# Optimization experiments

Measured on AMD Instinct MI355X. Metric: run time of the kernel, lower is better.

## Reference

```python
import math
import jax, jax.numpy as jnp
import numpy as np

C, NH, NL, NP, NLAYERS, FFN = 256, 8, 3, 4, 6, 1024
DH = C // NH
SHAPES = ((64, 64), (32, 32), (16, 16))  # (H,W) for res3, res4, res5
SIZES = [h * w for h, w in SHAPES]
STARTS = np.cumsum([0] + SIZES[:-1]).tolist()
EPS = 1e-5


def _sin_pe(H, W):
    d = C // 4
    y = jnp.arange(H, dtype=jnp.float32)[:, None]
    x = jnp.arange(W, dtype=jnp.float32)[None, :]
    div = jnp.exp(jnp.arange(d, dtype=jnp.float32) * (-math.log(10000.0) / d))[:, None, None]
    pe = jnp.concatenate([
        jnp.broadcast_to(jnp.sin(y * div), (d, H, W)),
        jnp.broadcast_to(jnp.cos(y * div), (d, H, W)),
        jnp.broadcast_to(jnp.sin(x * div), (d, H, W)),
        jnp.broadcast_to(jnp.cos(x * div), (d, H, W)),
    ], axis=0)  # (C,H,W)
    return pe.reshape(C, H * W).T  # (HW, C)


def _ref_points():
    pts = []
    for H, W in SHAPES:
        y = jnp.linspace(0.5 / H, 1.0 - 0.5 / H, H)
        x = jnp.linspace(0.5 / W, 1.0 - 0.5 / W, W)
        ry, rx = jnp.meshgrid(y, x, indexing='ij')
        pts.append(jnp.stack([rx.ravel(), ry.ravel()], -1))
    return jnp.concatenate(pts, 0)[None, :, None, :]  # (1,N,1,2), same per level


def _layernorm(x, g, b):
    mu = x.mean(-1, keepdims=True)
    v = ((x - mu) ** 2).mean(-1, keepdims=True)
    return (x - mu) * jax.lax.rsqrt(v + EPS) * g + b


def _bilinear(v, loc, H, W):
    # v: (B,HW,NH,DH); loc: (B,N,NH,NP,2) in [0,1]; grid_sample align_corners=False, zero pad
    B, N = loc.shape[0], loc.shape[1]
    x = loc[..., 0] * W - 0.5
    y = loc[..., 1] * H - 0.5
    x0 = jnp.floor(x); y0 = jnp.floor(y)
    wx = x - x0; wy = y - y0
    x0i = x0.astype(jnp.int32); y0i = y0.astype(jnp.int32)
    v_t = jnp.transpose(v, (0, 2, 1, 3))  # (B,NH,HW,DH)

    def corner(xi, yi, w):
        valid = (xi >= 0) & (xi < W) & (yi >= 0) & (yi < H)
        idx = jnp.clip(yi, 0, H - 1) * W + jnp.clip(xi, 0, W - 1)  # (B,N,NH,NP)
        idx = jnp.transpose(idx, (0, 2, 1, 3)).reshape(B, NH, N * NP)
        g = jnp.take_along_axis(v_t, idx[..., None], axis=2)  # (B,NH,N*NP,DH)
        g = g.reshape(B, NH, N, NP, DH).transpose(0, 2, 1, 3, 4)
        return g * (w * valid)[..., None]

    return (corner(x0i, y0i, (1 - wx) * (1 - wy))
            + corner(x0i + 1, y0i, wx * (1 - wy))
            + corner(x0i, y0i + 1, (1 - wx) * wy)
            + corner(x0i + 1, y0i + 1, wx * wy))


def _forward(res2, res3, res4, res5, level_embed, off_W, off_b, aw_W, aw_b, val_W, val_b,
             out_W, out_b, ln1_g, ln1_b, fc1_W, fc1_b, fc2_W, fc2_b, ln2_g, ln2_b,
             lat_W, lat_b, sm_W, sm_b, gn_g, gn_b):
    feats = [res3, res4, res5]
    B = res3.shape[0]
    flat = jnp.concatenate(
        [f.reshape(B, C, -1).transpose(0, 2, 1) + level_embed[i] for i, f in enumerate(feats)], 1)
    pe = jnp.concatenate([_sin_pe(H, W) for H, W in SHAPES], 0)[None]  # (1,N,C)
    ref = _ref_points()  # (1,N,1,2)
    normalizer = jnp.array([[W, H] for H, W in SHAPES], jnp.float32)  # (NL,2) as (W,H)
    N = flat.shape[1]

    x = flat
    for l in range(NLAYERS):
        q = x + pe
        value = (x @ val_W[l].T + val_b[l]).reshape(B, N, NH, DH)
        off = (q @ off_W[l].T + off_b[l]).reshape(B, N, NH, NL, NP, 2)
        aw = jax.nn.softmax((q @ aw_W[l].T + aw_b[l]).reshape(B, N, NH, NL * NP), -1)
        aw = aw.reshape(B, N, NH, NL, NP)
        loc = ref[:, :, None, :, None, :] + off / normalizer[None, None, None, :, None, :]
        attn = jnp.zeros((B, N, NH, DH), x.dtype)
        for li, (H, W) in enumerate(SHAPES):
            v_l = value[:, STARTS[li]:STARTS[li] + SIZES[li]]
            samp = _bilinear(v_l, loc[:, :, :, li], H, W)  # (B,N,NH,NP,DH)
            attn = attn + jnp.einsum('bnhpd,bnhp->bnhd', samp, aw[:, :, :, li])
        attn = attn.reshape(B, N, C) @ out_W[l].T + out_b[l]
        x = _layernorm(x + attn, ln1_g[l], ln1_b[l])
        h = jax.nn.relu(x @ fc1_W[l].T + fc1_b[l]) @ fc2_W[l].T + fc2_b[l]
        x = _layernorm(x + h, ln2_g[l], ln2_b[l])

    outs = []
    for li, (H, W) in enumerate(SHAPES):
        tok = x[:, STARTS[li]:STARTS[li] + SIZES[li]]
        outs.append(tok.transpose(0, 2, 1).reshape(B, C, H, W))
    o3, o4, o5 = outs

    r2_lat = jnp.einsum('bchw,oc->bohw', res2, lat_W) + lat_b[None, :, None, None]
    Hr, Wr = res2.shape[2], res2.shape[3]
    r3_up = jax.image.resize(o3, (B, C, Hr, Wr), method='bilinear')
    s = jax.lax.conv_general_dilated(r2_lat + r3_up, sm_W, (1, 1), ((1, 1), (1, 1)),
                                     dimension_numbers=('NCHW', 'OIHW', 'NCHW'))
    s = s + sm_b[None, :, None, None]
    # GroupNorm(32, C)
    g = s.reshape(B, 32, C // 32, Hr, Wr)
    mu = g.mean((2, 3, 4), keepdims=True)
    var = jnp.var(g, axis=(2, 3, 4), keepdims=True)
    g = (g - mu) * jax.lax.rsqrt(var + EPS)
    s = g.reshape(B, C, Hr, Wr) * gn_g[None, :, None, None] + gn_b[None, :, None, None]
    s = jax.nn.gelu(s, approximate=False)
    return s, o3, o4, o5


def setup_inputs() -> dict:
    key = jax.random.key(0)
    ks = jax.random.split(key, 16)
    def rn(k, shape, s=0.02):
        return jax.random.normal(k, shape, jnp.float32) * s
    B = 2
    L = NLAYERS
    return {
        'res2': jax.random.normal(ks[0], (B, C, 128, 128), jnp.float32),
        'res3': jax.random.normal(ks[1], (B, C, 64, 64), jnp.float32),
        'res4': jax.random.normal(ks[2], (B, C, 32, 32), jnp.float32),
        'res5': jax.random.normal(ks[3], (B, C, 16, 16), jnp.float32),
        'level_embed': rn(ks[4], (NL, C)),
        'off_W': rn(ks[5], (L, NH * NL * NP * 2, C)), 'off_b': jnp.zeros((L, NH * NL * NP * 2)),
        'aw_W': rn(ks[6], (L, NH * NL * NP, C)), 'aw_b': jnp.zeros((L, NH * NL * NP)),
        'val_W': rn(ks[7], (L, C, C)), 'val_b': jnp.zeros((L, C)),
        'out_W': rn(ks[8], (L, C, C)), 'out_b': jnp.zeros((L, C)),
        'ln1_g': jnp.ones((L, C)), 'ln1_b': jnp.zeros((L, C)),
        'fc1_W': rn(ks[9], (L, FFN, C)), 'fc1_b': jnp.zeros((L, FFN)),
        'fc2_W': rn(ks[10], (L, C, FFN)), 'fc2_b': jnp.zeros((L, C)),
        'ln2_g': jnp.ones((L, C)), 'ln2_b': jnp.zeros((L, C)),
        'lat_W': rn(ks[11], (C, C)), 'lat_b': jnp.zeros((C,)),
        'sm_W': rn(ks[12], (C, C, 3, 3)), 'sm_b': jnp.zeros((C,)),
        'gn_g': jnp.ones((C,)), 'gn_b': jnp.zeros((C,)),
    }


def reference(res2, res3, res4, res5, level_embed, off_W, off_b, aw_W, aw_b, val_W, val_b,
              out_W, out_b, ln1_g, ln1_b, fc1_W, fc1_b, fc2_W, fc2_b, ln2_g, ln2_b,
              lat_W, lat_b, sm_W, sm_b, gn_g, gn_b):
    return _forward(res2, res3, res4, res5, level_embed, off_W, off_b, aw_W, aw_b,
                    val_W, val_b, out_W, out_b, ln1_g, ln1_b, fc1_W, fc1_b, fc2_W, fc2_b,
                    ln2_g, ln2_b, lat_W, lat_b, sm_W, sm_b, gn_g, gn_b)
```

## Files before the change

### kernel.cpp

```cpp
#include <hip/hip_runtime.h>

namespace {
constexpr int Bn   = 2;
constexpr int Cc   = 256;
constexpr int Ntok = 5376;
constexpr int Ffn  = 1024;
constexpr int HW2  = 128 * 128;
constexpr float EPSf = 1e-5f;
constexpr int WL   = 729088;
}

typedef __attribute__((ext_vector_type(8))) short bf16x8;
typedef __attribute__((ext_vector_type(4))) float f32x4;

__device__ inline unsigned short f2bf(float x) {
  unsigned u = __float_as_uint(x);
  return (unsigned short)((u + 0x7fffu + ((u >> 16) & 1u)) >> 16);
}
__device__ inline float bf2f(unsigned short b) {
  return __uint_as_float((unsigned)b << 16);
}

__device__ inline void store_chunk_f32(unsigned short* lds, int row, int g,
                                       const float* v8) {
  int sg = g ^ (row & 7);
  unsigned short tmp[8];
#pragma unroll
  for (int j = 0; j < 8; j++) tmp[j] = f2bf(v8[j]);
  *reinterpret_cast<uint4*>(&lds[row * 64 + sg * 8]) =
      *reinterpret_cast<const uint4*>(tmp);
}
__device__ inline void store_chunk_bf(unsigned short* lds, int row, int g,
                                      uint4 v) {
  int sg = g ^ (row & 7);
  *reinterpret_cast<uint4*>(&lds[row * 64 + sg * 8]) = v;
}

__global__ __launch_bounds__(256) void wconv_all(
    const float* __restrict__ valW, const float* __restrict__ offW,
    const float* __restrict__ awW, const float* __restrict__ outW,
    const float* __restrict__ fc1W, const float* __restrict__ fc2W,
    unsigned short* __restrict__ wbf) {
  int i4 = blockIdx.x * 256 + threadIdx.x;
  if (i4 >= 1093632) return;
  int l = i4 / 182272;
  int e = (i4 - l * 182272) * 4;
  const float* src;
  int off;
  if (e < 65536) { src = valW + (size_t)l * 65536; off = e; }
  else if (e < 139264) {
    int j = e - 65536;
    if (j < 49152) { src = offW + (size_t)l * 49152; off = j; }
    else { src = awW + (size_t)l * 24576; off = j - 49152; }
  } else if (e < 204800) { src = outW + (size_t)l * 65536; off = e - 139264; }
  else if (e < 466944) { src = fc1W + (size_t)l * 262144; off = e - 204800; }
  else { src = fc2W + (size_t)l * 262144; off = e - 466944; }
  float4 v = *reinterpret_cast<const float4*>(&src[off]);
  unsigned short t[4] = {f2bf(v.x), f2bf(v.y), f2bf(v.z), f2bf(v.w)};
  *reinterpret_cast<uint2*>(&wbf[(size_t)l * WL + e]) =
      *reinterpret_cast<const uint2*>(t);
}

__global__ void wconv_flat(const float* __restrict__ src,
                           unsigned short* __restrict__ dst, int n4) {
  int i = blockIdx.x * 256 + threadIdx.x;
  if (i >= n4) return;
  float4 v = *reinterpret_cast<const float4*>(&src[i * 4]);
  unsigned short t[4] = {f2bf(v.x), f2bf(v.y), f2bf(v.z), f2bf(v.w)};
  *reinterpret_cast<uint2*>(&dst[i * 4]) = *reinterpret_cast<const uint2*>(t);
}

__global__ void pe_kernel(unsigned short* __restrict__ pe) {
  for (int i = blockIdx.x * blockDim.x + threadIdx.x; i < Ntok * Cc;
       i += gridDim.x * blockDim.x) {
    int c = i & 255;
    int p = i >> 8;
    int li = (p < 4096) ? 0 : ((p < 5120) ? 1 : 2);
    int start = (li == 0) ? 0 : ((li == 1) ? 4096 : 5120);
    int W = 64 >> li;
    int sp = p - start;
    int shift = 6 - li;
    int iy = sp >> shift;
    int ix = sp & (W - 1);
    int j = c & 63;
    int sel = c >> 6;
    float div = expf(-(float)j * (9.210340371976184f / 64.f));
    float coord = (sel < 2) ? (float)iy : (float)ix;
    float arg = coord * div;
    pe[i] = f2bf((sel & 1) ? cosf(arg) : sinf(arg));
  }
}

__global__ void flatten_kernel(const float* __restrict__ r3,
                               const float* __restrict__ r4,
                               const float* __restrict__ r5,
                               const float* __restrict__ lemb,
                               const unsigned short* __restrict__ peb,
                               float* __restrict__ x,
                               unsigned short* __restrict__ xb,
                               unsigned short* __restrict__ qb) {
  const int NPC = Ntok * Cc;
  for (int i = blockIdx.x * blockDim.x + threadIdx.x; i < Bn * NPC;
       i += gridDim.x * blockDim.x) {
    int c = i & 255;
    int rest = i >> 8;
    int p = rest % Ntok;
    int b = rest / Ntok;
    int li = (p < 4096) ? 0 : ((p < 5120) ? 1 : 2);
    int start = (li == 0) ? 0 : ((li == 1) ? 4096 : 5120);
    int size = (li == 0) ? 4096 : ((li == 1) ? 1024 : 256);
    const float* f = (li == 0) ? r3 : ((li == 1) ? r4 : r5);
    int sp = p - start;
    float v = f[((size_t)(b * Cc + c)) * size + sp] + lemb[li * Cc + c];
    x[i] = v;
    xb[i] = f2bf(v);
    qb[i] = f2bf(v + bf2f(peb[i - b * NPC]));
  }
}

template <int ACT, int OBF>
__global__ __launch_bounds__(256) void gemm_mfma_b(
    const unsigned short* __restrict__ A, const unsigned short* __restrict__ Wb,
    const float* __restrict__ bias, void* __restrict__ outp,
    int M, int N, int K, int nbx) {
  __shared__ unsigned short As[64 * 64];
  __shared__ unsigned short Ws[128 * 64];
  const int tid = threadIdx.x;
  const int nwg = gridDim.x;
  const int swz = (blockIdx.x & 7) * (nwg >> 3) + (blockIdx.x >> 3);
  const int m0 = (swz / nbx) * 64, n0 = (swz % nbx) * 128;
  const int wid = tid >> 6, lane = tid & 63;
  const int wm = wid >> 1, wn = wid & 1;
  const int lr = lane & 15, lh = lane >> 4;
  const int r8 = tid >> 3, g8 = tid & 7;
  f32x4 acc[2][4];
#pragma unroll
  for (int i = 0; i < 2; i++)
#pragma unroll
    for (int j = 0; j < 4; j++) acc[i][j] = f32x4{0.f, 0.f, 0.f, 0.f};

  uint4 ra[2], rw[4];
  const uint4 z4 = uint4{0, 0, 0, 0};
#pragma unroll
  for (int i = 0; i < 2; i++)
    ra[i] = *reinterpret_cast<const uint4*>(
        &A[(size_t)(m0 + r8 + i * 32) * K + g8 * 8]);
#pragma unroll
  for (int i = 0; i < 4; i++) {
    int n = n0 + r8 + i * 32;
    rw[i] = (n < N) ? *reinterpret_cast<const uint4*>(
                          &Wb[(size_t)n * K + g8 * 8])
                    : z4;
  }

  for (int k0 = 0; k0 < K; k0 += 64) {
    if (k0) __syncthreads();
#pragma unroll
    for (int i = 0; i < 2; i++) store_chunk_bf(As, r8 + i * 32, g8, ra[i]);
#pragma unroll
    for (int i = 0; i < 4; i++) store_chunk_bf(Ws, r8 + i * 32, g8, rw[i]);
    __syncthreads();
    int kn = k0 + 64;
    if (kn < K) {
#pragma unroll
      for (int i = 0; i < 2; i++)
        ra[i] = *reinterpret_cast<const uint4*>(
            &A[(size_t)(m0 + r8 + i * 32) * K + kn + g8 * 8]);
#pragma unroll
      for (int i = 0; i < 4; i++) {
        int n = n0 + r8 + i * 32;
        rw[i] = (n < N) ? *reinterpret_cast<const uint4*>(
                              &Wb[(size_t)n * K + kn + g8 * 8])
                        : z4;
      }
    }
    bf16x8 af[2][2], bfr[4][2];
#pragma unroll
    for (int mi = 0; mi < 2; mi++) {
      int r = wm * 32 + mi * 16 + lr;
#pragma unroll
      for (int s = 0; s < 2; s++) {
        int g = s * 4 + lh;
        af[mi][s] =
            *reinterpret_cast<const bf16x8*>(&As[r * 64 + (g ^ (r & 7)) * 8]);
      }
    }
#pragma unroll
    for (int nj = 0; nj < 4; nj++) {
      int r = wn * 64 + nj * 16 + lr;
#pragma unroll
      for (int s = 0; s < 2; s++) {
        int g = s * 4 + lh;
        bfr[nj][s] =
            *reinterpret_cast<const bf16x8*>(&Ws[r * 64 + (g ^ (r & 7)) * 8]);
      }
    }
#pragma unroll
    for (int mi = 0; mi < 2; mi++)
#pragma unroll
      for (int nj = 0; nj < 4; nj++) {
        acc[mi][nj] = __builtin_amdgcn_mfma_f32_16x16x32_bf16(
            af[mi][0], bfr[nj][0], acc[mi][nj], 0, 0, 0);
        acc[mi][nj] = __builtin_amdgcn_mfma_f32_16x16x32_bf16(
            af[mi][1], bfr[nj][1], acc[mi][nj], 0, 0, 0);
      }
  }
#pragma unroll
  for (int mi = 0; mi < 2; mi++) {
    int row = m0 + wm * 32 + mi * 16 + lh * 4;
#pragma unroll
    for (int nj = 0; nj < 4; nj++) {
      int col = n0 + wn * 64 + nj * 16 + lr;
      if (col >= N) continue;
      float b = bias[col];
#pragma unroll
      for (int r = 0; r < 4; r++) {
        float v = acc[mi][nj][r] + b;
        if (ACT) v = fmaxf(v, 0.f);
        if (OBF)
          ((unsigned short*)outp)[(size_t)(row + r) * N + col] = f2bf(v);
        else
          ((float*)outp)[(size_t)(row + r) * N + col] = v;
      }
    }
  }
}

template <int WRITEQ>
__global__ __launch_bounds__(256) void gemm_ln(
    const unsigned short* __restrict__ A, const unsigned short* __restrict__ Wb,
    const float* __restrict__ bias, const float* __restrict__ g,
    const float* __restrict__ bta, float* __restrict__ x,
    unsigned short* __restrict__ xb, const unsigned short* __restrict__ peb,
    unsigned short* __restrict__ qb, int K) {
  __shared__ unsigned short As[64 * 64];
  __shared__ unsigned short Ws[256 * 64];
  const int tid = threadIdx.x;
  const int swz = (blockIdx.x & 7) * 21 + (blockIdx.x >> 3);
  const int m0 = swz * 64;
  const int wid = tid >> 6, lane = tid & 63;
  const int lr = lane & 15, lh = lane >> 4;
  const int r8 = tid >> 3, g8 = tid & 7;
  f32x4 acc[16];
#pragma unroll
  for (int i = 0; i < 16; i++) acc[i] = f32x4{0.f, 0.f, 0.f, 0.f};

  uint4 ra[2], rw[8];
#pragma unroll
  for (int i = 0; i < 2; i++)
    ra[i] = *reinterpret_cast<const uint4*>(
        &A[(size_t)(m0 + r8 + i * 32) * K + g8 * 8]);
#pragma unroll
  for (int i = 0; i < 8; i++)
    rw[i] = *reinterpret_cast<const uint4*>(
        &Wb[(size_t)(r8 + i * 32) * K + g8 * 8]);

  for (int k0 = 0; k0 < K; k0 += 64) {
    if (k0) __syncthreads();
#pragma unroll
    for (int i = 0; i < 2; i++) store_chunk_bf(As, r8 + i * 32, g8, ra[i]);
#pragma unroll
    for (int i = 0; i < 8; i++) store_chunk_bf(Ws, r8 + i * 32, g8, rw[i]);
    __syncthreads();
    int kn = k0 + 64;
    if (kn < K) {
#pragma unroll
      for (int i = 0; i < 2; i++)
        ra[i] = *reinterpret_cast<const uint4*>(
            &A[(size_t)(m0 + r8 + i * 32) * K + kn + g8 * 8]);
#pragma unroll
      for (int i = 0; i < 8; i++)
        rw[i] = *reinterpret_cast<const uint4*>(
            &Wb[(size_t)(r8 + i * 32) * K + kn + g8 * 8]);
    }
    bf16x8 af[2];
    {
      int r = wid * 16 + lr;
#pragma unroll
      for (int s = 0; s < 2; s++) {
        int gg2 = s * 4 + lh;
        af[s] =
            *reinterpret_cast<const bf16x8*>(&As[r * 64 + (gg2 ^ (r & 7)) * 8]);
      }
    }
#pragma unroll
    for (int nt = 0; nt < 16; nt++) {
      int r = nt * 16 + lr;
      bf16x8 b0 =
          *reinterpret_cast<const bf16x8*>(&Ws[r * 64 + (lh ^ (r & 7)) * 8]);
      bf16x8 b1 = *reinterpret_cast<const bf16x8*>(
          &Ws[r * 64 + ((4 + lh) ^ (r & 7)) * 8]);
      acc[nt] =
          __builtin_amdgcn_mfma_f32_16x16x32_bf16(af[0], b0, acc[nt], 0, 0, 0);
      acc[nt] =
          __builtin_amdgcn_mfma_f32_16x16x32_bf16(af[1], b1, acc[nt], 0, 0, 0);
    }
  }

  const int rowl = wid * 16 + lh * 4;
#pragma unroll
  for (int nt = 0; nt < 16; nt++) {
    int col = nt * 16 + lr;
    float bs = bias[col];
#pragma unroll
    for (int r = 0; r < 4; r++)
      acc[nt][r] += bs + x[(size_t)(m0 + rowl + r) * 256 + col];
  }
  float mu[4], rstd[4];
#pragma unroll
  for (int r = 0; r < 4; r++) {
    float s = 0.f;
#pragma unroll
    for (int nt = 0; nt < 16; nt++) s += acc[nt][r];
#pragma unroll
    for (int o = 8; o > 0; o >>= 1) s += __shfl_xor(s, o);
    mu[r] = s * (1.f / 256.f);
  }
#pragma unroll
  for (int r = 0; r < 4; r++) {
    float q = 0.f;
#pragma unroll
    for (int nt = 0; nt < 16; nt++) {
      float d = acc[nt][r] - mu[r];
      q += d * d;
    }
#pragma unroll
    for (int o = 8; o > 0; o >>= 1) q += __shfl_xor(q, o);
    rstd[r] = rsqrtf(q * (1.f / 256.f) + EPSf);
  }
#pragma unroll
  for (int nt = 0; nt < 16; nt++) {
    int col = nt * 16 + lr;
    float gw = g[col], bw = bta[col];
#pragma unroll
    for (int r = 0; r < 4; r++) {
      int row = m0 + rowl + r;
      size_t idx = (size_t)row * 256 + col;
      float o = (acc[nt][r] - mu[r]) * rstd[r] * gw + bw;
      x[idx] = o;
      xb[idx] = f2bf(o);
      if (WRITEQ) {
        size_t pc = idx - (row >= Ntok ? (size_t)Ntok * 256 : 0);
        qb[idx] = f2bf(o + bf2f(peb[pc]));
      }
    }
  }
}

__global__ __launch_bounds__(256) void gemm_head(
    const unsigned short* __restrict__ xb, const unsigned short* __restrict__ qb,
    const unsigned short* __restrict__ wv, const unsigned short* __restrict__ wo,
    const float* __restrict__ valB, const float* __restrict__ offB,
    const float* __restrict__ awB, unsigned short* __restrict__ valO,
    float* __restrict__ offO, float* __restrict__ awO) {
  __shared__ unsigned short As[64 * 64];
  __shared__ unsigned short Ws[128 * 64];
  const int tid = threadIdx.x;
  const int swz = (blockIdx.x & 7) * 105 + (blockIdx.x >> 3);
  const bool isval = swz < 336;
  const unsigned short* A;
  const unsigned short* W;
  int m0, n0, Nn;
  if (isval) {
    A = xb; W = wv; Nn = 256;
    m0 = (swz >> 1) * 64; n0 = (swz & 1) * 128;
  } else {
    int s = swz - 336;
    A = qb; W = wo; Nn = 288;
    m0 = (s / 3) * 64; n0 = (s % 3) * 128;
  }
  const int wid = tid >> 6, lane = tid & 63;
  const int wm = wid >> 1, wn = wid & 1;
  const int lr = lane & 15, lh = lane >> 4;
  const int r8 = tid >> 3, g8 = tid & 7;
  f32x4 acc[2][4];
#pragma unroll
  for (int i = 0; i < 2; i++)
#pragma unroll
    for (int j = 0; j < 4; j++) acc[i][j] = f32x4{0.f, 0.f, 0.f, 0.f};

  uint4 ra[2], rw[4];
  const uint4 z4 = uint4{0, 0, 0, 0};
#pragma unroll
  for (int i = 0; i < 2; i++)
    ra[i] = *reinterpret_cast<const uint4*>(
        &A[(size_t)(m0 + r8 + i * 32) * 256 + g8 * 8]);
#pragma unroll
  for (int i = 0; i < 4; i++) {
    int n = n0 + r8 + i * 32;
    rw[i] = (n < Nn) ? *reinterpret_cast<const uint4*>(
                           &W[(size_t)n * 256 + g8 * 8])
                     : z4;
  }

  for (int k0 = 0; k0 < 256; k0 += 64) {
    if (k0) __syncthreads();
#pragma unroll
    for (int i = 0; i < 2; i++) store_chunk_bf(As, r8 + i * 32, g8, ra[i]);
#pragma unroll
    for (int i = 0; i < 4; i++) store_chunk_bf(Ws, r8 + i * 32, g8, rw[i]);
    __syncthreads();
    int kn = k0 + 64;
    if (kn < 256) {
#pragma unroll
      for (int i = 0; i < 2; i++)
        ra[i] = *reinterpret_cast<const uint4*>(
            &A[(size_t)(m0 + r8 + i * 32) * 256 + kn + g8 * 8]);
#pragma unroll
      for (int i = 0; i < 4; i++) {
        int n = n0 + r8 + i * 32;
        rw[i] = (n < Nn) ? *reinterpret_cast<const uint4*>(
                               &W[(size_t)n * 256 + kn + g8 * 8])
                         : z4;
      }
    }
    bf16x8 af[2][2], bfr[4][2];
#pragma unroll
    for (int mi = 0; mi < 2; mi++) {
      int r = wm * 32 + mi * 16 + lr;
#pragma unroll
      for (int s = 0; s < 2; s++) {
        int g = s * 4 + lh;
        af[mi][s] =
            *reinterpret_cast<const bf16x8*>(&As[r * 64 + (g ^ (r & 7)) * 8]);
      }
    }
#pragma unroll
    for (int nj = 0; nj < 4; nj++) {
      int r = wn * 64 + nj * 16 + lr;
#pragma unroll
      for (int s = 0; s < 2; s++) {
        int g = s * 4 + lh;
        bfr[nj][s] =
            *reinterpret_cast<const bf16x8*>(&Ws[r * 64 + (g ^ (r & 7)) * 8]);
      }
    }
#pragma unroll
    for (int mi = 0; mi < 2; mi++)
#pragma unroll
      for (int nj = 0; nj < 4; nj++) {
        acc[mi][nj] = __builtin_amdgcn_mfma_f32_16x16x32_bf16(
            af[mi][0], bfr[nj][0], acc[mi][nj], 0, 0, 0);
        acc[mi][nj] = __builtin_amdgcn_mfma_f32_16x16x32_bf16(
            af[mi][1], bfr[nj][1], acc[mi][nj], 0, 0, 0);
      }
  }
#pragma unroll
  for (int mi = 0; mi < 2; mi++) {
    int row = m0 + wm * 32 + mi * 16 + lh * 4;
#pragma unroll
    for (int nj = 0; nj < 4; nj++) {
      int col = n0 + wn * 64 + nj * 16 + lr;
      if (isval) {
        float b = valB[col];
#pragma unroll
        for (int r = 0; r < 4; r++)
          valO[(size_t)(row + r) * 256 + col] = f2bf(acc[mi][nj][r] + b);
      } else {
        if (col >= 288) continue;
        float b = (col < 192) ? offB[col] : awB[col - 192];
#pragma unroll
        for (int r = 0; r < 4; r++) {
          float v = acc[mi][nj][r] + b;
          if (col < 192)
            offO[(size_t)(row + r) * 192 + col] = v;
          else
            awO[(size_t)(row + r) * 96 + col - 192] = v;
        }
      }
    }
  }
}

__global__ __launch_bounds__(256) void msda_fused(
    const unsigned short* __restrict__ value, const float* __restrict__ off,
    const float* __restrict__ awl, unsigned short* __restrict__ attn) {
  __shared__ int recI[8][12][4];
  __shared__ float recW[8][12][4];
  const int tid = threadIdx.x;
  if (tid < 96) {
    int gq = tid / 12;
    int p = tid - gq * 12;
    int gid = blockIdx.x * 8 + gq;
    int h = gid & 7;
    int bn = gid >> 3;
    int n = bn % Ntok;
    int b = bn / Ntok;
    int li0 = (n < 4096) ? 0 : ((n < 5120) ? 1 : 2);
    int start0 = (li0 == 0) ? 0 : ((li0 == 1) ? 4096 : 5120);
    int shift = 6 - li0;
    int Wn = 1 << shift;
    int sp = n - start0;
    int iy = sp >> shift;
    int ix = sp & (Wn - 1);
    float refx = (ix + 0.5f) / (float)Wn;
    float refy = (iy + 0.5f) / (float)Wn;
    const float* ap = awl + (size_t)bn * 96 + h * 12;
    float lg[12];
    float mx = -1e30f;
#pragma unroll
    for (int j = 0; j < 12; j++) { lg[j] = ap[j]; mx = fmaxf(mx, lg[j]); }
    float ssum = 0.f;
#pragma unroll
    for (int j = 0; j < 12; j++) { lg[j] = expf(lg[j] - mx); ssum += lg[j]; }
    float w = lg[p] / ssum;
    int li = p >> 2;
    int HWl = 64 >> li;
    int st = (li == 0) ? 0 : ((li == 1) ? 4096 : 5120);
    const float* op = off + (size_t)bn * 192 + h * 24;
    float ox = op[p * 2 + 0];
    float oy = op[p * 2 + 1];
    float lx = refx + ox / (float)HWl;
    float ly = refy + oy / (float)HWl;
    float fx = lx * (float)HWl - 0.5f;
    float fy = ly * (float)HWl - 0.5f;
    float x0f = floorf(fx), y0f = floorf(fy);
    float wx = fx - x0f, wy = fy - y0f;
    int ix0 = (int)x0f, iy0 = (int)y0f;
    int base = (b * Ntok + st) * 256 + h * 32;
#pragma unroll
    for (int cr = 0; cr < 4; cr++) {
      int cx = ix0 + (cr & 1);
      int cy = iy0 + (cr >> 1);
      bool valid = (cx >= 0) & (cx < HWl) & (cy >= 0) & (cy < HWl);
      float wc = ((cr & 1) ? wx : 1.f - wx) * ((cr >> 1) ? wy : 1.f - wy);
      int cxc = min(max(cx, 0), HWl - 1);
      int cyc = min(max(cy, 0), HWl - 1);
      recI[gq][p][cr] = base + (cyc * HWl + cxc) * 256;
      recW[gq][p][cr] = valid ? (w * wc) : 0.f;
    }
  }
  __syncthreads();
  const int grp = tid >> 5, lane = tid & 31;
  const unsigned short* vb = value + lane;
  float acc = 0.f;
#pragma unroll
  for (int p = 0; p < 12; p++) {
    int4 idx = *reinterpret_cast<const int4*>(&recI[grp][p][0]);
    float4 w = *reinterpret_cast<const float4*>(&recW[grp][p][0]);
    acc += w.x * bf2f(vb[idx.x]);
    acc += w.y * bf2f(vb[idx.y]);
    acc += w.z * bf2f(vb[idx.z]);
    acc += w.w * bf2f(vb[idx.w]);
  }
  int gid = blockIdx.x * 8 + grp;
  attn[(size_t)gid * 32 + lane] = f2bf(acc);
}

__global__ __launch_bounds__(256) void conv3x3_mfma(
    const unsigned short* __restrict__ T, const unsigned short* __restrict__ Wt,
    const float* __restrict__ bias, unsigned short* __restrict__ out) {
  __shared__ unsigned short As[2][64 * 64];
  __shared__ unsigned short Ws[2][128 * 64];
  const int tid = threadIdx.x;
  const int nwg = gridDim.x;
  const int swz = (blockIdx.x & 7) * (nwg >> 3) + (blockIdx.x >> 3);
  const int m0 = (swz >> 1) * 64, n0 = (swz & 1) * 128;
  const int b = m0 >> 14;
  const int p0 = m0 & 16383;
  const int y = p0 >> 7;
  const int x0 = p0 & 127;
  const int wid = tid >> 6, lane = tid & 63;
  const int wm = wid >> 1, wn = wid & 1;
  const int lr = lane & 15, lh = lane >> 4;
  const int r8 = tid >> 3, g8 = tid & 7;
  f32x4 acc[2][4];
#pragma unroll
  for (int i = 0; i < 2; i++)
#pragma unroll
    for (int j = 0; j < 4; j++) acc[i][j] = f32x4{0.f, 0.f, 0.f, 0.f};

  uint4 ra[2], rw[4];
  auto loadA = [&](int kc, uint4* r) {
    int tap = kc >> 2;
    int cb = (kc & 3) * 64;
    int dy = tap / 3 - 1, dx = tap % 3 - 1;
    int yy = y + dy;
#pragma unroll
    for (int i = 0; i < 2; i++) {
      int row = r8 + i * 32;
      int xx = x0 + row + dx;
      uint4 v = uint4{0, 0, 0, 0};
      if (yy >= 0 && yy < 128 && xx >= 0 && xx < 128)
        v = *reinterpret_cast<const uint4*>(
            &T[((size_t)(b * 16384 + yy * 128 + xx)) * 256 + cb + g8 * 8]);
      r[i] = v;
    }
  };
  auto loadW = [&](int kc, uint4* r) {
#pragma unroll
    for (int i = 0; i < 4; i++)
      r[i] = *reinterpret_cast<const uint4*>(
          &Wt[(size_t)(n0 + r8 + i * 32) * 2304 + kc * 64 + g8 * 8]);
  };
  loadA(0, ra);
  loadW(0, rw);

  for (int kc = 0; kc < 36; kc++) {
    const int pb = kc & 1;
#pragma unroll
    for (int i = 0; i < 2; i++) store_chunk_bf(As[pb], r8 + i * 32, g8, ra[i]);
#pragma unroll
    for (int i = 0; i < 4; i++) store_chunk_bf(Ws[pb], r8 + i * 32, g8, rw[i]);
    __syncthreads();
    if (kc + 1 < 36) {
      loadA(kc + 1, ra);
      loadW(kc + 1, rw);
    }
    bf16x8 af[2][2], bfr[4][2];
#pragma unroll
    for (int mi = 0; mi < 2; mi++) {
      int r = wm * 32 + mi * 16 + lr;
#pragma unroll
      for (int s = 0; s < 2; s++) {
        int g = s * 4 + lh;
        af[mi][s] = *reinterpret_cast<const bf16x8*>(
            &As[pb][r * 64 + (g ^ (r & 7)) * 8]);
      }
    }
#pragma unroll
    for (int nj = 0; nj < 4; nj++) {
      int r = wn * 64 + nj * 16 + lr;
#pragma unroll
      for (int s = 0; s < 2; s++) {
        int g = s * 4 + lh;
        bfr[nj][s] = *reinterpret_cast<const bf16x8*>(
            &Ws[pb][r * 64 + (g ^ (r & 7)) * 8]);
      }
    }
#pragma unroll
    for (int mi = 0; mi < 2; mi++)
#pragma unroll
      for (int nj = 0; nj < 4; nj++) {
        acc[mi][nj] = __builtin_amdgcn_mfma_f32_16x16x32_bf16(
            af[mi][0], bfr[nj][0], acc[mi][nj], 0, 0, 0);
        acc[mi][nj] = __builtin_amdgcn_mfma_f32_16x16x32_bf16(
            af[mi][1], bfr[nj][1], acc[mi][nj], 0, 0, 0);
      }
  }
#pragma unroll
  for (int mi = 0; mi < 2; mi++) {
    int row = m0 + wm * 32 + mi * 16 + lh * 4;
#pragma unroll
    for (int nj = 0; nj < 4; nj++) {
      int col = n0 + wn * 64 + nj * 16 + lr;
      float b = bias[col];
#pragma unroll
      for (int r = 0; r < 4; r++)
        out[(size_t)(row + r) * 256 + col] = f2bf(acc[mi][nj][r] + b);
    }
  }
}

__global__ __launch_bounds__(256) void gemm_tn_mfma(
    const float* __restrict__ A, const unsigned short* __restrict__ Wb,
    const float* __restrict__ bias, unsigned short* __restrict__ out) {
  __shared__ unsigned short As[64 * 64];
  __shared__ unsigned short Ws[128 * 64];
  const int tid = threadIdx.x;
  const int nwg = gridDim.x;
  const int swz = (blockIdx.x & 7) * (nwg >> 3) + (blockIdx.x >> 3);
  const int m0 = (swz >> 1) * 64, n0 = (swz & 1) * 128;
  const int b = m0 >> 14;
  const int p0 = m0 & 16383;
  const int wid = tid >> 6, lane = tid & 63;
  const int wm = wid >> 1, wn = wid & 1;
  const int lr = lane & 15, lh = lane >> 4;
  const int r8 = tid >> 3, g8 = tid & 7;
  const int arow = tid & 63, agb = tid >> 6;
  f32x4 acc[2][4];
#pragma unroll
  for (int i = 0; i < 2; i++)
#pragma unroll
    for (int j = 0; j < 4; j++) acc[i][j] = f32x4{0.f, 0.f, 0.f, 0.f};

  float va[16];
  uint4 rw[4];
  auto loadA = [&](int k0, float* v) {
#pragma unroll
    for (int i = 0; i < 2; i++) {
      int g = agb + i * 4;
#pragma unroll
      for (int j = 0; j < 8; j++)
        v[i * 8 + j] =
            A[(size_t)(b * 256 + k0 + g * 8 + j) * 16384 + p0 + arow];
    }
  };
  auto loadW = [&](int k0, uint4* r) {
#pragma unroll
    for (int i = 0; i < 4; i++)
      r[i] = *reinterpret_cast<const uint4*>(
          &Wb[(size_t)(n0 + r8 + i * 32) * 256 + k0 + g8 * 8]);
  };
  loadA(0, va);
  loadW(0, rw);

  for (int k0 = 0; k0 < 256; k0 += 64) {
    if (k0) __syncthreads();
#pragma unroll
    for (int i = 0; i < 2; i++)
      store_chunk_f32(As, arow, agb + i * 4, &va[i * 8]);
#pragma unroll
    for (int i = 0; i < 4; i++) store_chunk_bf(Ws, r8 + i * 32, g8, rw[i]);
    __syncthreads();
    int kn = k0 + 64;
    if (kn < 256) {
      loadA(kn, va);
      loadW(kn, rw);
    }
    bf16x8 af[2][2], bfr[4][2];
#pragma unroll
    for (int mi = 0; mi < 2; mi++) {
      int r = wm * 32 + mi * 16 + lr;
#pragma unroll
      for (int s = 0; s < 2; s++) {
        int g = s * 4 + lh;
        af[mi][s] =
            *reinterpret_cast<const bf16x8*>(&As[r * 64 + (g ^ (r & 7)) * 8]);
      }
    }
#pragma unroll
    for (int nj = 0; nj < 4; nj++) {
      int r = wn * 64 + nj * 16 + lr;
#pragma unroll
      for (int s = 0; s < 2; s++) {
        int g = s * 4 + lh;
        bfr[nj][s] =
            *reinterpret_cast<const bf16x8*>(&Ws[r * 64 + (g ^ (r & 7)) * 8]);
      }
    }
#pragma unroll
    for (int mi = 0; mi < 2; mi++)
#pragma unroll
      for (int nj = 0; nj < 4; nj++) {
        acc[mi][nj] = __builtin_amdgcn_mfma_f32_16x16x32_bf16(
            af[mi][0], bfr[nj][0], acc[mi][nj], 0, 0, 0);
        acc[mi][nj] = __builtin_amdgcn_mfma_f32_16x16x32_bf16(
            af[mi][1], bfr[nj][1], acc[mi][nj], 0, 0, 0);
      }
  }
#pragma unroll
  for (int mi = 0; mi < 2; mi++) {
    int row = m0 + wm * 32 + mi * 16 + lh * 4;
#pragma unroll
    for (int nj = 0; nj < 4; nj++) {
      int col = n0 + wn * 64 + nj * 16 + lr;
      float b = bias[col];
#pragma unroll
      for (int r = 0; r < 4; r++)
        out[(size_t)(row + r) * 256 + col] = f2bf(acc[mi][nj][r] + b);
    }
  }
}

__global__ __launch_bounds__(256) void upsample_add(
    const float* __restrict__ xrows, unsigned short* __restrict__ t) {
  int bp = blockIdx.x;
  int c = threadIdx.x;
  int b = bp >> 14;
  int p = bp & 16383;
  int Y = p >> 7, X = p & 127;
  float yc = Y * 0.5f - 0.25f;
  float y0f = floorf(yc);
  float wy = yc - y0f;
  int y0 = (int)y0f, y1 = y0 + 1;
  int y0c = min(max(y0, 0), 63), y1c = min(max(y1, 0), 63);
  float xc = X * 0.5f - 0.25f;
  float x0f = floorf(xc);
  float wx = xc - x0f;
  int xq0 = (int)x0f, xq1 = xq0 + 1;
  int x0c = min(max(xq0, 0), 63), x1c = min(max(xq1, 0), 63);
  const float* base = xrows + (size_t)b * Ntok * 256;
  float v00 = base[(size_t)(y0c * 64 + x0c) * 256 + c];
  float v01 = base[(size_t)(y0c * 64 + x1c) * 256 + c];
  float v10 = base[(size_t)(y1c * 64 + x0c) * 256 + c];
  float v11 = base[(size_t)(y1c * 64 + x1c) * 256 + c];
  float v = (1.f - wy) * ((1.f - wx) * v00 + wx * v01) +
            wy * ((1.f - wx) * v10 + wx * v11);
  size_t idx = (size_t)bp * 256 + c;
  t[idx] = f2bf(bf2f(t[idx]) + v);
}

__global__ void rows3_to_nchw(const float* __restrict__ xrows,
                              float* __restrict__ o3, float* __restrict__ o4,
                              float* __restrict__ o5) {
  __shared__ float tile[32][33];
  int bx = blockIdx.x;
  int start, size, pblk;
  float* out;
  if (bx < 128) { start = 0; size = 4096; pblk = bx; out = o3; }
  else if (bx < 160) { start = 4096; size = 1024; pblk = bx - 128; out = o4; }
  else { start = 5120; size = 256; pblk = bx - 160; out = o5; }
  int p0 = pblk * 32, c0 = blockIdx.y * 32, b = blockIdx.z;
  int tx = threadIdx.x, tyy = threadIdx.y;
  for (int i = tyy; i < 32; i += 8)
    tile[i][tx] = xrows[((size_t)(b * Ntok + start + p0 + i)) * 256 + c0 + tx];
  __syncthreads();
  for (int i = tyy; i < 32; i += 8)
    out[((size_t)(b * 256 + c0 + i)) * size + p0 + tx] = tile[tx][i];
}

__global__ void wt_transpose(const float* __restrict__ w,
                             unsigned short* __restrict__ wt) {
  for (int i = blockIdx.x * blockDim.x + threadIdx.x; i < 256 * 2304;
       i += gridDim.x * blockDim.x) {
    int o = i / 2304;
    int r = i % 2304;
    int tap = r >> 8;
    int c = r & 255;
    wt[i] = f2bf(w[((size_t)(o * 256 + c)) * 9 + tap]);
  }
}

__global__ __launch_bounds__(256) void gn_partial(
    const unsigned short* __restrict__ s, float* __restrict__ part) {
  int blk = blockIdx.x;
  int pr = blk & 15;
  int bg = blk >> 4;
  int g = bg & 31;
  int b = bg >> 5;
  int tid = threadIdx.x;
  float sum = 0.f, sq = 0.f;
  for (int e = pr * 8192 + tid; e < (pr + 1) * 8192; e += 256) {
    int p = e >> 3, cc = e & 7;
    float v = bf2f(s[((size_t)(b * 16384 + p)) * 256 + g * 8 + cc]);
    sum += v;
    sq += v * v;
  }
  __shared__ float rs[256], rq[256];
  rs[tid] = sum;
  rq[tid] = sq;
  __syncthreads();
  for (int st = 128; st > 0; st >>= 1) {
    if (tid < st) { rs[tid] += rs[tid + st]; rq[tid] += rq[tid + st]; }
    __syncthreads();
  }
  if (tid == 0) {
    part[(size_t)blk * 2 + 0] = rs[0];
    part[(size_t)blk * 2 + 1] = rq[0];
  }
}

__global__ void gn_final(const float* __restrict__ part,
                         float* __restrict__ stats) {
  int tid = threadIdx.x;
  if (tid < 64) {
    float s = 0.f, q = 0.f;
    for (int j = 0; j < 16; j++) {
      s += part[(size_t)(tid * 16 + j) * 2 + 0];
      q += part[(size_t)(tid * 16 + j) * 2 + 1];
    }
    float mu = s * (1.f / 131072.f);
    float var = q * (1.f / 131072.f) - mu * mu;
    stats[tid * 2 + 0] = mu;
    stats[tid * 2 + 1] = rsqrtf(var + EPSf);
  }
}

__global__ void gn_apply(const unsigned short* __restrict__ s,
                         const float* __restrict__ stats,
                         const float* __restrict__ gg,
                         const float* __restrict__ gb,
                         float* __restrict__ out) {
  __shared__ float tile[32][33];
  int p0 = blockIdx.x * 32, c0 = blockIdx.y * 32, b = blockIdx.z;
  int tx = threadIdx.x, tyy = threadIdx.y;
  int c = c0 + tx;
  float mu = stats[(b * 32 + (c >> 3)) * 2 + 0];
  float rstd = stats[(b * 32 + (c >> 3)) * 2 + 1];
  float gw = gg[c], bw = gb[c];
  for (int i = tyy; i < 32; i += 8) {
    float v = bf2f(s[((size_t)(b * 16384 + p0 + i)) * 256 + c]);
    v = (v - mu) * rstd * gw + bw;
    v = 0.5f * v * (1.f + erff(v * 0.70710678118654752f));
    tile[i][tx] = v;
  }
  __syncthreads();
  for (int i = tyy; i < 32; i += 8)
    out[((size_t)(b * 256 + c0 + i)) * 16384 + p0 + tx] = tile[tx][i];
}

extern "C" void kernel_launch(void* const* d_in, const int* in_sizes, int n_in,
                              void* d_out, int out_size, void* d_ws,
                              size_t ws_size, hipStream_t stream) {
  (void)in_sizes; (void)n_in; (void)out_size; (void)ws_size;
  const float* res2  = (const float*)d_in[0];
  const float* res3  = (const float*)d_in[1];
  const float* res4  = (const float*)d_in[2];
  const float* res5  = (const float*)d_in[3];
  const float* lemb  = (const float*)d_in[4];
  const float* off_W = (const float*)d_in[5];
  const float* off_b = (const float*)d_in[6];
  const float* aw_W  = (const float*)d_in[7];
  const float* aw_b  = (const float*)d_in[8];
  const float* val_W = (const float*)d_in[9];
  const float* val_b = (const float*)d_in[10];
  const float* out_W = (const float*)d_in[11];
  const float* out_b = (const float*)d_in[12];
  const float* ln1_g = (const float*)d_in[13];
  const float* ln1_b = (const float*)d_in[14];
  const float* fc1_W = (const float*)d_in[15];
  const float* fc1_b = (const float*)d_in[16];
  const float* fc2_W = (const float*)d_in[17];
  const float* fc2_b = (const float*)d_in[18];
  const float* ln2_g = (const float*)d_in[19];
  const float* ln2_b = (const float*)d_in[20];
  const float* lat_W = (const float*)d_in[21];
  const float* lat_b = (const float*)d_in[22];
  const float* sm_W  = (const float*)d_in[23];
  const float* sm_b  = (const float*)d_in[24];
  const float* gn_g  = (const float*)d_in[25];
  const float* gn_b  = (const float*)d_in[26];

  float* ws = (float*)d_ws;
  float*          x      = ws;
  unsigned short* xb     = (unsigned short*)(ws + 2752512);
  unsigned short* peb    = (unsigned short*)(ws + 4128768);
  unsigned short* qb     = (unsigned short*)(ws + 4816896);
  unsigned short* valueb = (unsigned short*)(ws + 6193152);
  float*          offb   = ws + 7569408;
  float*          awl    = ws + 9633792;
  unsigned short* attnb  = (unsigned short*)(ws + 10665984);
  float*          tmp    = ws + 12042240;
  unsigned short* hb     = (unsigned short*)(ws + 14794752);
  unsigned short* tbuf   = hb;
  unsigned short* wtbuf  = (unsigned short*)(ws + 20299776);
  float*          gnpart = ws + 20594688;
  float*          gnstat = ws + 20596736;
  unsigned short* wbf    = (unsigned short*)(ws + 20596864);
  unsigned short* wlat   = wbf + (size_t)6 * WL;
  unsigned short* sbufb  = (unsigned short*)ws;
  (void)tmp;

  float* out_s  = (float*)d_out;
  float* out_o3 = out_s + (size_t)Bn * Cc * HW2;
  float* out_o4 = out_o3 + (size_t)Bn * Cc * 4096;
  float* out_o5 = out_o4 + (size_t)Bn * Cc * 1024;

  const int M = Bn * Ntok;

  pe_kernel<<<1024, 256, 0, stream>>>(peb);
  flatten_kernel<<<1024, 256, 0, stream>>>(res3, res4, res5, lemb, peb, x, xb,
                                           qb);
  wconv_all<<<4272, 256, 0, stream>>>(val_W, off_W, aw_W, out_W, fc1_W, fc2_W,
                                      wbf);
  wconv_flat<<<64, 256, 0, stream>>>(lat_W, wlat, 16384);
  wt_transpose<<<1024, 256, 0, stream>>>(sm_W, wtbuf);

  for (int l = 0; l < 6; l++) {
    const unsigned short* wl = wbf + (size_t)l * WL;
    gemm_head<<<840, 256, 0, stream>>>(
        xb, qb, wl + 0, wl + 65536, val_b + l * 256, off_b + l * 192,
        aw_b + l * 96, valueb, offb, awl);
    msda_fused<<<10752, 256, 0, stream>>>(valueb, offb, awl, attnb);
    gemm_ln<0><<<168, 256, 0, stream>>>(
        attnb, wl + 139264, out_b + l * 256, ln1_g + l * 256, ln1_b + l * 256,
        x, xb, peb, qb, 256);
    gemm_mfma_b<1, 1><<<1344, 256, 0, stream>>>(
        xb, wl + 204800, fc1_b + l * 1024, hb, M, 1024, 256, 8);
    gemm_ln<1><<<168, 256, 0, stream>>>(
        hb, wl + 466944, fc2_b + l * 256, ln2_g + l * 256, ln2_b + l * 256,
        x, xb, peb, qb, 1024);
  }

  rows3_to_nchw<<<dim3(168, 8, 2), dim3(32, 8), 0, stream>>>(x, out_o3, out_o4,
                                                             out_o5);

  gemm_tn_mfma<<<1024, 256, 0, stream>>>(res2, wlat, lat_b, tbuf);
  upsample_add<<<32768, 256, 0, stream>>>(x, tbuf);
  conv3x3_mfma<<<1024, 256, 0, stream>>>(tbuf, wtbuf, sm_b, sbufb);
  gn_partial<<<1024, 256, 0, stream>>>(sbufb, gnpart);
  gn_final<<<1, 64, 0, stream>>>(gnpart, gnstat);
  gn_apply<<<dim3(512, 8, 2), dim3(32, 8), 0, stream>>>(sbufb, gnstat, gn_g,
                                                        gn_b, out_s);
}
```

Before: 766.1 us.

## Retile gemm_ln and conv3x3, fuse upsample-add into lateral GEMM epilogue

gemm_ln now uses 32-row tiles with a 2x2 warp split and cross-warp LDS reductions for the layernorm statistics, doubling the grid to 336 blocks for better CU occupancy. conv3x3 switches to full 256-column tiles over a single LDS buffer, so each A tile is loaded once instead of twice, at the cost of dropping double buffering. The separate upsample_add kernel is removed and its bilinear upsample-and-add is folded into the gemm_tn_mfma epilogue, saving a launch and a read-modify-write pass over tbuf.

Result: faster. 750.6 us (-2.0%).

```diff
diff --git a/kernel.cpp b/kernel.cpp
--- a/kernel.cpp
+++ b/kernel.cpp
@@ -233,23 +233,23 @@
     const float* __restrict__ bta, float* __restrict__ x,
     unsigned short* __restrict__ xb, const unsigned short* __restrict__ peb,
     unsigned short* __restrict__ qb, int K) {
-  __shared__ unsigned short As[64 * 64];
+  __shared__ unsigned short As[32 * 64];
   __shared__ unsigned short Ws[256 * 64];
+  __shared__ float pred[2][2][16];
+  __shared__ float qred[2][2][16];
   const int tid = threadIdx.x;
-  const int swz = (blockIdx.x & 7) * 21 + (blockIdx.x >> 3);
-  const int m0 = swz * 64;
+  const int swz = (blockIdx.x & 7) * 42 + (blockIdx.x >> 3);
+  const int m0 = swz * 32;
   const int wid = tid >> 6, lane = tid & 63;
+  const int wm = wid >> 1, wn = wid & 1;
   const int lr = lane & 15, lh = lane >> 4;
   const int r8 = tid >> 3, g8 = tid & 7;
-  f32x4 acc[16];
-#pragma unroll
-  for (int i = 0; i < 16; i++) acc[i] = f32x4{0.f, 0.f, 0.f, 0.f};
-
-  uint4 ra[2], rw[8];
-#pragma unroll
-  for (int i = 0; i < 2; i++)
-    ra[i] = *reinterpret_cast<const uint4*>(
-        &A[(size_t)(m0 + r8 + i * 32) * K + g8 * 8]);
+  f32x4 acc[8];
+#pragma unroll
+  for (int i = 0; i < 8; i++) acc[i] = f32x4{0.f, 0.f, 0.f, 0.f};
+
+  uint4 ra, rw[8];
+  ra = *reinterpret_cast<const uint4*>(&A[(size_t)(m0 + r8) * K + g8 * 8]);
 #pragma unroll
   for (int i = 0; i < 8; i++)
     rw[i] = *reinterpret_cast<const uint4*>(
@@ -257,17 +257,14 @@
 
   for (int k0 = 0; k0 < K; k0 += 64) {
     if (k0) __syncthreads();
-#pragma unroll
-    for (int i = 0; i < 2; i++) store_chunk_bf(As, r8 + i * 32, g8, ra[i]);
+    store_chunk_bf(As, r8, g8, ra);
 #pragma unroll
     for (int i = 0; i < 8; i++) store_chunk_bf(Ws, r8 + i * 32, g8, rw[i]);
     __syncthreads();
     int kn = k0 + 64;
     if (kn < K) {
-#pragma unroll
-      for (int i = 0; i < 2; i++)
-        ra[i] = *reinterpret_cast<const uint4*>(
-            &A[(size_t)(m0 + r8 + i * 32) * K + kn + g8 * 8]);
+      ra = *reinterpret_cast<const uint4*>(
+          &A[(size_t)(m0 + r8) * K + kn + g8 * 8]);
 #pragma unroll
       for (int i = 0; i < 8; i++)
         rw[i] = *reinterpret_cast<const uint4*>(
@@ -275,7 +272,7 @@
     }
     bf16x8 af[2];
     {
-      int r = wid * 16 + lr;
+      int r = wm * 16 + lr;
 #pragma unroll
       for (int s = 0; s < 2; s++) {
         int gg2 = s * 4 + lh;
@@ -284,8 +281,8 @@
       }
     }
 #pragma unroll
-    for (int nt = 0; nt < 16; nt++) {
-      int r = nt * 16 + lr;
+    for (int nt = 0; nt < 8; nt++) {
+      int r = wn * 128 + nt * 16 + lr;
       bf16x8 b0 =
           *reinterpret_cast<const bf16x8*>(&Ws[r * 64 + (lh ^ (r & 7)) * 8]);
       bf16x8 b1 = *reinterpret_cast<const bf16x8*>(
@@ -297,40 +294,61 @@
     }
   }
 
-  const int rowl = wid * 16 + lh * 4;
-#pragma unroll
-  for (int nt = 0; nt < 16; nt++) {
-    int col = nt * 16 + lr;
+  const int rowl = wm * 16 + lh * 4;
+#pragma unroll
+  for (int nt = 0; nt < 8; nt++) {
+    int col = wn * 128 + nt * 16 + lr;
     float bs = bias[col];
 #pragma unroll
     for (int r = 0; r < 4; r++)
       acc[nt][r] += bs + x[(size_t)(m0 + rowl + r) * 256 + col];
   }
-  float mu[4], rstd[4];
+  float sum[4];
 #pragma unroll
   for (int r = 0; r < 4; r++) {
     float s = 0.f;
 #pragma unroll
-    for (int nt = 0; nt < 16; nt++) s += acc[nt][r];
+    for (int nt = 0; nt < 8; nt++) s += acc[nt][r];
 #pragma unroll
     for (int o = 8; o > 0; o >>= 1) s += __shfl_xor(s, o);
-    mu[r] = s * (1.f / 256.f);
-  }
+    sum[r] = s;
+  }
+  if (lr == 0) {
+#pragma unroll
+    for (int r = 0; r < 4; r++) pred[wm][wn][lh * 4 + r] = sum[r];
+  }
+  __syncthreads();
+  float mu[4];
+#pragma unroll
+  for (int r = 0; r < 4; r++)
+    mu[r] = (pred[wm][0][lh * 4 + r] + pred[wm][1][lh * 4 + r]) * (1.f / 256.f);
+  float qs[4];
 #pragma unroll
   for (int r = 0; r < 4; r++) {
     float q = 0.f;
 #pragma unroll
-    for (int nt = 0; nt < 16; nt++) {
+    for (int nt = 0; nt < 8; nt++) {
       float d = acc[nt][r] - mu[r];
       q += d * d;
     }
 #pragma unroll
     for (int o = 8; o > 0; o >>= 1) q += __shfl_xor(q, o);
-    rstd[r] = rsqrtf(q * (1.f / 256.f) + EPSf);
-  }
-#pragma unroll
-  for (int nt = 0; nt < 16; nt++) {
-    int col = nt * 16 + lr;
+    qs[r] = q;
+  }
+  if (lr == 0) {
+#pragma unroll
+    for (int r = 0; r < 4; r++) qred[wm][wn][lh * 4 + r] = qs[r];
+  }
+  __syncthreads();
+  float rstd[4];
+#pragma unroll
+  for (int r = 0; r < 4; r++)
+    rstd[r] = rsqrtf(
+        (qred[wm][0][lh * 4 + r] + qred[wm][1][lh * 4 + r]) * (1.f / 256.f) +
+        EPSf);
+#pragma unroll
+  for (int nt = 0; nt < 8; nt++) {
+    int col = wn * 128 + nt * 16 + lr;
     float gw = g[col], bw = bta[col];
 #pragma unroll
     for (int r = 0; r < 4; r++) {
@@ -550,27 +568,23 @@
 __global__ __launch_bounds__(256) void conv3x3_mfma(
     const unsigned short* __restrict__ T, const unsigned short* __restrict__ Wt,
     const float* __restrict__ bias, unsigned short* __restrict__ out) {
-  __shared__ unsigned short As[2][64 * 64];
-  __shared__ unsigned short Ws[2][128 * 64];
+  __shared__ unsigned short As[64 * 64];
+  __shared__ unsigned short Ws[256 * 64];
   const int tid = threadIdx.x;
-  const int nwg = gridDim.x;
-  const int swz = (blockIdx.x & 7) * (nwg >> 3) + (blockIdx.x >> 3);
-  const int m0 = (swz >> 1) * 64, n0 = (swz & 1) * 128;
+  const int swz = (blockIdx.x & 7) * 64 + (blockIdx.x >> 3);
+  const int m0 = swz * 64;
   const int b = m0 >> 14;
   const int p0 = m0 & 16383;
   const int y = p0 >> 7;
   const int x0 = p0 & 127;
   const int wid = tid >> 6, lane = tid & 63;
-  const int wm = wid >> 1, wn = wid & 1;
   const int lr = lane & 15, lh = lane >> 4;
   const int r8 = tid >> 3, g8 = tid & 7;
-  f32x4 acc[2][4];
-#pragma unroll
-  for (int i = 0; i < 2; i++)
-#pragma unroll
-    for (int j = 0; j < 4; j++) acc[i][j] = f32x4{0.f, 0.f, 0.f, 0.f};
-
-  uint4 ra[2], rw[4];
+  f32x4 acc[16];
+#pragma unroll
+  for (int i = 0; i < 16; i++) acc[i] = f32x4{0.f, 0.f, 0.f, 0.f};
+
+  uint4 ra[2], rw[8];
   auto loadA = [&](int kc, uint4* r) {
     int tap = kc >> 2;
     int cb = (kc & 3) * 64;
@@ -589,72 +603,62 @@
   };
   auto loadW = [&](int kc, uint4* r) {
 #pragma unroll
-    for (int i = 0; i < 4; i++)
+    for (int i = 0; i < 8; i++)
       r[i] = *reinterpret_cast<const uint4*>(
-          &Wt[(size_t)(n0 + r8 + i * 32) * 2304 + kc * 64 + g8 * 8]);
+          &Wt[(size_t)(r8 + i * 32) * 2304 + kc * 64 + g8 * 8]);
   };
   loadA(0, ra);
   loadW(0, rw);
 
   for (int kc = 0; kc < 36; kc++) {
-    const int pb = kc & 1;
-#pragma unroll
-    for (int i = 0; i < 2; i++) store_chunk_bf(As[pb], r8 + i * 32, g8, ra[i]);
-#pragma unroll
-    for (int i = 0; i < 4; i++) store_chunk_bf(Ws[pb], r8 + i * 32, g8, rw[i]);
+    if (kc) __syncthreads();
+#pragma unroll
+    for (int i = 0; i < 2; i++) store_chunk_bf(As, r8 + i * 32, g8, ra[i]);
+#pragma unroll
+    for (int i = 0; i < 8; i++) store_chunk_bf(Ws, r8 + i * 32, g8, rw[i]);
     __syncthreads();
     if (kc + 1 < 36) {
       loadA(kc + 1, ra);
       loadW(kc + 1, rw);
     }
-    bf16x8 af[2][2], bfr[4][2];
-#pragma unroll
-    for (int mi = 0; mi < 2; mi++) {
-      int r = wm * 32 + mi * 16 + lr;
+    bf16x8 af[2];
+    {
+      int r = wid * 16 + lr;
 #pragma unroll
       for (int s = 0; s < 2; s++) {
-        int g = s * 4 + lh;
-        af[mi][s] = *reinterpret_cast<const bf16x8*>(
-            &As[pb][r * 64 + (g ^ (r & 7)) * 8]);
-      }
-    }
-#pragma unroll
-    for (int nj = 0; nj < 4; nj++) {
-      int r = wn * 64 + nj * 16 + lr;
-#pragma unroll
-      for (int s = 0; s < 2; s++) {
-        int g = s * 4 + lh;
-        bfr[nj][s] = *reinterpret_cast<const bf16x8*>(
-            &Ws[pb][r * 64 + (g ^ (r & 7)) * 8]);
-      }
-    }
-#pragma unroll
-    for (int mi = 0; mi < 2; mi++)
-#pragma unroll
-      for (int nj = 0; nj < 4; nj++) {
-        acc[mi][nj] = __builtin_amdgcn_mfma_f32_16x16x32_bf16(
-            af[mi][0], bfr[nj][0], acc[mi][nj], 0, 0, 0);
-        acc[mi][nj] = __builtin_amdgcn_mfma_f32_16x16x32_bf16(
-            af[mi][1], bfr[nj][1], acc[mi][nj], 0, 0, 0);
-      }
-  }
-#pragma unroll
-  for (int mi = 0; mi < 2; mi++) {
-    int row = m0 + wm * 32 + mi * 16 + lh * 4;
-#pragma unroll
-    for (int nj = 0; nj < 4; nj++) {
-      int col = n0 + wn * 64 + nj * 16 + lr;
-      float b = bias[col];
-#pragma unroll
-      for (int r = 0; r < 4; r++)
-        out[(size_t)(row + r) * 256 + col] = f2bf(acc[mi][nj][r] + b);
-    }
+        int gg2 = s * 4 + lh;
+        af[s] =
+            *reinterpret_cast<const bf16x8*>(&As[r * 64 + (gg2 ^ (r & 7)) * 8]);
+      }
+    }
+#pragma unroll
+    for (int nt = 0; nt < 16; nt++) {
+      int r = nt * 16 + lr;
+      bf16x8 b0 =
+          *reinterpret_cast<const bf16x8*>(&Ws[r * 64 + (lh ^ (r & 7)) * 8]);
+      bf16x8 b1 = *reinterpret_cast<const bf16x8*>(
+          &Ws[r * 64 + ((4 + lh) ^ (r & 7)) * 8]);
+      acc[nt] =
+          __builtin_amdgcn_mfma_f32_16x16x32_bf16(af[0], b0, acc[nt], 0, 0, 0);
+      acc[nt] =
+          __builtin_amdgcn_mfma_f32_16x16x32_bf16(af[1], b1, acc[nt], 0, 0, 0);
+    }
+  }
+  const int rowl = wid * 16 + lh * 4;
+#pragma unroll
+  for (int nt = 0; nt < 16; nt++) {
+    int col = nt * 16 + lr;
+    float bs = bias[col];
+#pragma unroll
+    for (int r = 0; r < 4; r++)
+      out[(size_t)(m0 + rowl + r) * 256 + col] = f2bf(acc[nt][r] + bs);
   }
 }
 
 __global__ __launch_bounds__(256) void gemm_tn_mfma(
     const float* __restrict__ A, const unsigned short* __restrict__ Wb,
-    const float* __restrict__ bias, unsigned short* __restrict__ out) {
+    const float* __restrict__ bias, const float* __restrict__ x,
+    unsigned short* __restrict__ out) {
   __shared__ unsigned short As[64 * 64];
   __shared__ unsigned short Ws[128 * 64];
   const int tid = threadIdx.x;
@@ -739,46 +743,38 @@
             af[mi][1], bfr[nj][1], acc[mi][nj], 0, 0, 0);
       }
   }
+  const float* xbse = x + (size_t)b * Ntok * 256;
 #pragma unroll
   for (int mi = 0; mi < 2; mi++) {
-    int row = m0 + wm * 32 + mi * 16 + lh * 4;
-#pragma unroll
-    for (int nj = 0; nj < 4; nj++) {
-      int col = n0 + wn * 64 + nj * 16 + lr;
-      float b = bias[col];
-#pragma unroll
-      for (int r = 0; r < 4; r++)
-        out[(size_t)(row + r) * 256 + col] = f2bf(acc[mi][nj][r] + b);
-    }
-  }
-}
-
-__global__ __launch_bounds__(256) void upsample_add(
-    const float* __restrict__ xrows, unsigned short* __restrict__ t) {
-  int bp = blockIdx.x;
-  int c = threadIdx.x;
-  int b = bp >> 14;
-  int p = bp & 16383;
-  int Y = p >> 7, X = p & 127;
-  float yc = Y * 0.5f - 0.25f;
-  float y0f = floorf(yc);
-  float wy = yc - y0f;
-  int y0 = (int)y0f, y1 = y0 + 1;
-  int y0c = min(max(y0, 0), 63), y1c = min(max(y1, 0), 63);
-  float xc = X * 0.5f - 0.25f;
-  float x0f = floorf(xc);
-  float wx = xc - x0f;
-  int xq0 = (int)x0f, xq1 = xq0 + 1;
-  int x0c = min(max(xq0, 0), 63), x1c = min(max(xq1, 0), 63);
-  const float* base = xrows + (size_t)b * Ntok * 256;
-  float v00 = base[(size_t)(y0c * 64 + x0c) * 256 + c];
-  float v01 = base[(size_t)(y0c * 64 + x1c) * 256 + c];
-  float v10 = base[(size_t)(y1c * 64 + x0c) * 256 + c];
-  float v11 = base[(size_t)(y1c * 64 + x1c) * 256 + c];
-  float v = (1.f - wy) * ((1.f - wx) * v00 + wx * v01) +
-            wy * ((1.f - wx) * v10 + wx * v11);
-  size_t idx = (size_t)bp * 256 + c;
-  t[idx] = f2bf(bf2f(t[idx]) + v);
+    int row0 = m0 + wm * 32 + mi * 16 + lh * 4;
+#pragma unroll
+    for (int r = 0; r < 4; r++) {
+      int p = (row0 + r) & 16383;
+      int Y = p >> 7, X = p & 127;
+      float yc = Y * 0.5f - 0.25f;
+      float y0f = floorf(yc);
+      float wy = yc - y0f;
+      int y0 = (int)y0f;
+      int y0c = min(max(y0, 0), 63), y1c = min(max(y0 + 1, 0), 63);
+      float xc = X * 0.5f - 0.25f;
+      float x0f = floorf(xc);
+      float wx = xc - x0f;
+      int xq0 = (int)x0f;
+      int x0c = min(max(xq0, 0), 63), x1c = min(max(xq0 + 1, 0), 63);
+      const float* r00 = xbse + (size_t)(y0c * 64 + x0c) * 256;
+      const float* r01 = xbse + (size_t)(y0c * 64 + x1c) * 256;
+      const float* r10 = xbse + (size_t)(y1c * 64 + x0c) * 256;
+      const float* r11 = xbse + (size_t)(y1c * 64 + x1c) * 256;
+#pragma unroll
+      for (int nj = 0; nj < 4; nj++) {
+        int col = n0 + wn * 64 + nj * 16 + lr;
+        float up = (1.f - wy) * ((1.f - wx) * r00[col] + wx * r01[col]) +
+                   wy * ((1.f - wx) * r10[col] + wx * r11[col]);
+        out[(size_t)(row0 + r) * 256 + col] =
+            f2bf(acc[mi][nj][r] + bias[col] + up);
+      }
+    }
+  }
 }
 
 __global__ void rows3_to_nchw(const float* __restrict__ xrows,
@@ -921,7 +917,6 @@
   float*          offb   = ws + 7569408;
   float*          awl    = ws + 9633792;
   unsigned short* attnb  = (unsigned short*)(ws + 10665984);
-  float*          tmp    = ws + 12042240;
   unsigned short* hb     = (unsigned short*)(ws + 14794752);
   unsigned short* tbuf   = hb;
   unsigned short* wtbuf  = (unsigned short*)(ws + 20299776);
@@ -930,7 +925,6 @@
   unsigned short* wbf    = (unsigned short*)(ws + 20596864);
   unsigned short* wlat   = wbf + (size_t)6 * WL;
   unsigned short* sbufb  = (unsigned short*)ws;
-  (void)tmp;
 
   float* out_s  = (float*)d_out;
   float* out_o3 = out_s + (size_t)Bn * Cc * HW2;
@@ -953,12 +947,12 @@
         xb, qb, wl + 0, wl + 65536, val_b + l * 256, off_b + l * 192,
         aw_b + l * 96, valueb, offb, awl);
     msda_fused<<<10752, 256, 0, stream>>>(valueb, offb, awl, attnb);
-    gemm_ln<0><<<168, 256, 0, stream>>>(
+    gemm_ln<0><<<336, 256, 0, stream>>>(
         attnb, wl + 139264, out_b + l * 256, ln1_g + l * 256, ln1_b + l * 256,
         x, xb, peb, qb, 256);
     gemm_mfma_b<1, 1><<<1344, 256, 0, stream>>>(
         xb, wl + 204800, fc1_b + l * 1024, hb, M, 1024, 256, 8);
-    gemm_ln<1><<<168, 256, 0, stream>>>(
+    gemm_ln<1><<<336, 256, 0, stream>>>(
         hb, wl + 466944, fc2_b + l * 256, ln2_g + l * 256, ln2_b + l * 256,
         x, xb, peb, qb, 1024);
   }
@@ -966,9 +960,8 @@
   rows3_to_nchw<<<dim3(168, 8, 2), dim3(32, 8), 0, stream>>>(x, out_o3, out_o4,
                                                              out_o5);
 
-  gemm_tn_mfma<<<1024, 256, 0, stream>>>(res2, wlat, lat_b, tbuf);
-  upsample_add<<<32768, 256, 0, stream>>>(x, tbuf);
-  conv3x3_mfma<<<1024, 256, 0, stream>>>(tbuf, wtbuf, sm_b, sbufb);
+  gemm_tn_mfma<<<1024, 256, 0, stream>>>(res2, wlat, lat_b, x, tbuf);
+  conv3x3_mfma<<<512, 256, 0, stream>>>(tbuf, wtbuf, sm_b, sbufb);
   gn_partial<<<1024, 256, 0, stream>>>(sbufb, gnpart);
   gn_final<<<1, 64, 0, stream>>>(gnpart, gnstat);
   gn_apply<<<dim3(512, 8, 2), dim3(32, 8), 0, stream>>>(sbufb, gnstat, gn_g,
```
